# Optimization experiments

Hardware: AMD Instinct MI355X
Metric: run time of the kernel (lower is better)

## Reference

```python
import jax, jax.numpy as jnp
import numpy as np


def _to_class(x):
    # x: (B, T, 1) -> class in {0,1,2,3}: (<0)->0, [0,1)->1, [1,2)->2, (>=2)->3
    return (jnp.clip(jnp.floor(x[..., 0]), -1.0, 2.0) + 1.0).astype(jnp.int32)


def setup_inputs() -> dict:
    key = jax.random.key(0)
    k1, k2, k3 = jax.random.split(key, 3)
    B, T = 524288, 48
    pred = jax.random.normal(k1, (B, T, 1), dtype=jnp.float32) * 1.5
    true = jax.random.normal(k2, (B, T, 1), dtype=jnp.float32) * 1.5
    score_matrix = jax.random.uniform(k3, (4, 4), dtype=jnp.float32) * 3.0
    return {"pred": pred, "true": true, "score_matrix": score_matrix}


def reference(pred, true, score_matrix):
    # normalize exp(-S) over all 16 entries
    e = jnp.exp(-score_matrix)
    sm = e / jnp.sum(e)  # (4, 4)
    pred_cls = _to_class(pred)  # (B, T) int32
    true_cls = _to_class(true)  # (B, T) int32
    gmgs_weight = sm[true_cls, pred_cls]  # (B, T) gather into 4x4 table
    sq = jnp.square(pred - true)[..., 0]  # (B, T)
    loss = jnp.sum(sq * gmgs_weight) / pred.shape[0]
    return loss
```

## Files before the change

### kernel.cpp

```cpp
#include <hip/hip_runtime.h>

#define BLOCK 256
#define GRID 2048

__device__ __forceinline__ float gmgs_term(float pv, float tv, const float* __restrict__ sm_e) {
    float pf = fminf(fmaxf(floorf(pv), -1.0f), 2.0f);
    float tf = fminf(fmaxf(floorf(tv), -1.0f), 2.0f);
    int pc = (int)pf + 1;
    int tc = (int)tf + 1;
    float d = pv - tv;
    return d * d * sm_e[tc * 4 + pc];
}

__device__ __forceinline__ float gmgs_quad(float4 p, float4 t, const float* __restrict__ sm_e) {
    return (gmgs_term(p.x, t.x, sm_e) + gmgs_term(p.y, t.y, sm_e))
         + (gmgs_term(p.z, t.z, sm_e) + gmgs_term(p.w, t.w, sm_e));
}

__global__ __launch_bounds__(BLOCK) void gmgs_loss_kernel(
    const float* __restrict__ pred,
    const float* __restrict__ tru,
    const float* __restrict__ score,
    float* __restrict__ out,
    int n4, int rem, float invB)
{
    __shared__ float sm_e[16];
    __shared__ float sred[BLOCK / 64];

    const int tid = threadIdx.x;
    if (tid < 16) sm_e[tid] = expf(-score[tid]);
    __syncthreads();

    const float4* __restrict__ pred4 = (const float4*)pred;
    const float4* __restrict__ tru4  = (const float4*)tru;

    const int stride = GRID * BLOCK;
    int i = (int)blockIdx.x * BLOCK + tid;
    float acc0 = 0.0f, acc1 = 0.0f, acc2 = 0.0f, acc3 = 0.0f;

    for (; i + 3 * stride < n4; i += 4 * stride) {
        float4 p0 = pred4[i];
        float4 p1 = pred4[i + stride];
        float4 p2 = pred4[i + 2 * stride];
        float4 p3 = pred4[i + 3 * stride];
        float4 t0 = tru4[i];
        float4 t1 = tru4[i + stride];
        float4 t2 = tru4[i + 2 * stride];
        float4 t3 = tru4[i + 3 * stride];
        acc0 += gmgs_quad(p0, t0, sm_e);
        acc1 += gmgs_quad(p1, t1, sm_e);
        acc2 += gmgs_quad(p2, t2, sm_e);
        acc3 += gmgs_quad(p3, t3, sm_e);
    }
    for (; i < n4; i += stride)
        acc0 += gmgs_quad(pred4[i], tru4[i], sm_e);

    if (blockIdx.x == 0 && tid < rem) {
        int j = n4 * 4 + tid;
        acc0 += gmgs_term(pred[j], tru[j], sm_e);
    }

    float acc = (acc0 + acc1) + (acc2 + acc3);
    #pragma unroll
    for (int off = 32; off > 0; off >>= 1)
        acc += __shfl_down(acc, off, 64);

    if ((tid & 63) == 0) sred[tid >> 6] = acc;
    __syncthreads();
    if (tid == 0) {
        float s = 0.0f;
        #pragma unroll
        for (int w = 0; w < BLOCK / 64; ++w) s += sred[w];
        float e = 0.0f;
        #pragma unroll
        for (int k = 0; k < 16; ++k) e += sm_e[k];
        atomicAdd(out, s * invB / e);
    }
}

extern "C" void kernel_launch(void* const* d_in, const int* in_sizes, int n_in,
                              void* d_out, int out_size, void* d_ws, size_t ws_size,
                              hipStream_t stream) {
    const float* pred  = (const float*)d_in[0];
    const float* tru   = (const float*)d_in[1];
    const float* score = (const float*)d_in[2];
    float* out = (float*)d_out;

    long long n = (long long)in_sizes[0];
    int n4  = (int)(n >> 2);
    int rem = (int)(n & 3);
    long long B = n / 48;
    float invB = 1.0f / (float)B;

    hipMemsetAsync(d_out, 0, sizeof(float), stream);
    gmgs_loss_kernel<<<GRID, BLOCK, 0, stream>>>(pred, tru, score, out, n4, rem, invB);
}
```

Before: 218.7 us.

## Replace grid-stride loop with one-shot blocks issuing all loads up front

```diff
diff --git a/kernel.cpp b/kernel.cpp
--- a/kernel.cpp
+++ b/kernel.cpp
@@ -1,15 +1,13 @@
 #include <hip/hip_runtime.h>
 
 #define BLOCK 256
-#define GRID 2048
+#define PAIRS 4
 
 __device__ __forceinline__ float gmgs_term(float pv, float tv, const float* __restrict__ sm_e) {
-    float pf = fminf(fmaxf(floorf(pv), -1.0f), 2.0f);
-    float tf = fminf(fmaxf(floorf(tv), -1.0f), 2.0f);
-    int pc = (int)pf + 1;
-    int tc = (int)tf + 1;
+    int pc = (int)fminf(fmaxf(floorf(pv), -1.0f), 2.0f) + 1;
+    int tc = (int)fminf(fmaxf(floorf(tv), -1.0f), 2.0f) + 1;
     float d = pv - tv;
-    return d * d * sm_e[tc * 4 + pc];
+    return d * d * sm_e[(tc << 2) | pc];
 }
 
 __device__ __forceinline__ float gmgs_quad(float4 p, float4 t, const float* __restrict__ sm_e) {
@@ -17,7 +15,9 @@
          + (gmgs_term(p.z, t.z, sm_e) + gmgs_term(p.w, t.w, sm_e));
 }
 
-__global__ __launch_bounds__(BLOCK) void gmgs_loss_kernel(
+__global__ __launch_bounds__(BLOCK, 4) void gmgs_loss_kernel(
+    const float4* __restrict__ pred4,
+    const float4* __restrict__ tru4,
     const float* __restrict__ pred,
     const float* __restrict__ tru,
     const float* __restrict__ score,
@@ -27,54 +27,46 @@
     __shared__ float sm_e[16];
     __shared__ float sred[BLOCK / 64];
 
-    const int tid = threadIdx.x;
+    const int tid  = threadIdx.x;
+    const int base = (int)blockIdx.x * (BLOCK * PAIRS) + tid;
+
+    float4 p[PAIRS], t[PAIRS];
+    bool inb[PAIRS];
+    #pragma unroll
+    for (int j = 0; j < PAIRS; ++j) {
+        int i = base + j * BLOCK;
+        inb[j] = (i < n4);
+        int ic = inb[j] ? i : 0;
+        p[j] = pred4[ic];
+        t[j] = tru4[ic];
+    }
+
     if (tid < 16) sm_e[tid] = expf(-score[tid]);
     __syncthreads();
 
-    const float4* __restrict__ pred4 = (const float4*)pred;
-    const float4* __restrict__ tru4  = (const float4*)tru;
-
-    const int stride = GRID * BLOCK;
-    int i = (int)blockIdx.x * BLOCK + tid;
-    float acc0 = 0.0f, acc1 = 0.0f, acc2 = 0.0f, acc3 = 0.0f;
-
-    for (; i + 3 * stride < n4; i += 4 * stride) {
-        float4 p0 = pred4[i];
-        float4 p1 = pred4[i + stride];
-        float4 p2 = pred4[i + 2 * stride];
-        float4 p3 = pred4[i + 3 * stride];
-        float4 t0 = tru4[i];
-        float4 t1 = tru4[i + stride];
-        float4 t2 = tru4[i + 2 * stride];
-        float4 t3 = tru4[i + 3 * stride];
-        acc0 += gmgs_quad(p0, t0, sm_e);
-        acc1 += gmgs_quad(p1, t1, sm_e);
-        acc2 += gmgs_quad(p2, t2, sm_e);
-        acc3 += gmgs_quad(p3, t3, sm_e);
-    }
-    for (; i < n4; i += stride)
-        acc0 += gmgs_quad(pred4[i], tru4[i], sm_e);
+    float acc = 0.0f;
+    #pragma unroll
+    for (int j = 0; j < PAIRS; ++j)
+        if (inb[j]) acc += gmgs_quad(p[j], t[j], sm_e);
 
     if (blockIdx.x == 0 && tid < rem) {
-        int j = n4 * 4 + tid;
-        acc0 += gmgs_term(pred[j], tru[j], sm_e);
+        int jj = n4 * 4 + tid;
+        acc += gmgs_term(pred[jj], tru[jj], sm_e);
     }
 
-    float acc = (acc0 + acc1) + (acc2 + acc3);
     #pragma unroll
     for (int off = 32; off > 0; off >>= 1)
         acc += __shfl_down(acc, off, 64);
-
     if ((tid & 63) == 0) sred[tid >> 6] = acc;
     __syncthreads();
     if (tid == 0) {
         float s = 0.0f;
         #pragma unroll
         for (int w = 0; w < BLOCK / 64; ++w) s += sred[w];
-        float e = 0.0f;
+        float z = 0.0f;
         #pragma unroll
-        for (int k = 0; k < 16; ++k) e += sm_e[k];
-        atomicAdd(out, s * invB / e);
+        for (int k = 0; k < 16; ++k) z += sm_e[k];
+        atomicAdd(out, s * invB / z);
     }
 }
 
@@ -92,6 +84,9 @@
     long long B = n / 48;
     float invB = 1.0f / (float)B;
 
+    int nblk = (n4 + BLOCK * PAIRS - 1) / (BLOCK * PAIRS);
+
     hipMemsetAsync(d_out, 0, sizeof(float), stream);
-    gmgs_loss_kernel<<<GRID, BLOCK, 0, stream>>>(pred, tru, score, out, n4, rem, invB);
+    gmgs_loss_kernel<<<nblk, BLOCK, 0, stream>>>(
+        (const float4*)pred, (const float4*)tru, pred, tru, score, out, n4, rem, invB);
 }
```

Measured after the change: 233.4 us. +6.7%, slower.
